# Performance work log

Hardware: AMD Instinct MI355X
Metric: run time of the kernel (lower is better)

## Reference

```python
import jax, jax.numpy as jnp
import numpy as np

K = 1024          # num_embeddings
D = 128           # embedding_dim
EMA_DECAY = 0.99
EPS = 1e-5


def setup_inputs() -> dict:
    key = jax.random.key(0)
    k1, k2, k3 = jax.random.split(key, 3)
    z = jax.random.normal(k1, (64, D, 32, 32), dtype=jnp.float32)
    codebook = jax.random.normal(k2, (K, D), dtype=jnp.float32)
    ema_count = jnp.zeros((K,), dtype=jnp.float32)
    ema_weight = jax.random.normal(k3, (K, D), dtype=jnp.float32)
    return {"z": z, "codebook": codebook, "ema_count": ema_count, "ema_weight": ema_weight}


def reference(z, codebook, ema_count, ema_weight):
    B, C, H, W = z.shape
    # flatten to [N, D] in BHWC order (matches permute(0,2,3,1).view(-1, D))
    z_flat = jnp.transpose(z, (0, 2, 3, 1)).reshape(-1, D)  # [N, D]

    # squared euclidean distances [N, K]
    distances = (
        jnp.sum(z_flat * z_flat, axis=1, keepdims=True)
        + jnp.sum(codebook * codebook, axis=1)
        - 2.0 * jnp.matmul(z_flat, codebook.T)
    )
    indices = jnp.argmin(distances, axis=1)  # [N] int

    # gather instead of one-hot @ codebook (same math)
    quantized_flat = codebook[indices]  # [N, D]
    # NOTE: faithful to original: raw view of BHWC-ordered flat buffer into z.shape
    quantized = quantized_flat.reshape(z.shape)

    # EMA statistics (no_grad in original): segment sums instead of one-hot matmuls
    encodings_sum = jax.ops.segment_sum(jnp.ones_like(indices, dtype=jnp.float32), indices, num_segments=K)
    dw = jax.ops.segment_sum(z_flat, indices, num_segments=K)  # [K, D]
    new_ema_count = EMA_DECAY * ema_count + (1.0 - EMA_DECAY) * encodings_sum
    new_ema_weight = EMA_DECAY * ema_weight + (1.0 - EMA_DECAY) * dw
    n = jnp.sum(new_ema_count)
    weights = (new_ema_count + EPS) / (n + K * EPS) * n
    new_codebook = new_ema_weight / weights[:, None]

    commitment_loss = jnp.mean((jax.lax.stop_gradient(quantized) - z) ** 2)
    codebook_loss = jnp.mean((quantized - jax.lax.stop_gradient(z)) ** 2)

    # straight-through estimator
    quantized_st = z + jax.lax.stop_gradient(quantized - z)

    idx_map = indices.reshape(B, H, W)
    return (quantized_st, idx_map, commitment_loss, codebook_loss,
            new_codebook, new_ema_count, new_ema_weight)
```

## Files before the change

kernel.cpp:

```cpp
#include <hip/hip_runtime.h>

#define NVEC 65536
#define KCB  1024
#define DIM  128
#define HW   1024
#define CHUNK 32
#define NCHUNKS (NVEC / CHUNK)

typedef __bf16 b16;
typedef b16 b16x8 __attribute__((ext_vector_type(8)));
typedef float f32x16 __attribute__((ext_vector_type(16)));

static __device__ __forceinline__ unsigned short f2bf(float f) {
  unsigned int x = __float_as_uint(f);
  unsigned int r = x + 0x7fffu + ((x >> 16) & 1u);
  return (unsigned short)(r >> 16);
}

__global__ void k_prep(const float* __restrict__ cb, const float* __restrict__ emw,
                       uint4* __restrict__ cbt, float* __restrict__ ccb,
                       double* __restrict__ cc64, float* __restrict__ out6,
                       int* __restrict__ hist, int* __restrict__ done) {
  const int t = blockIdx.x * blockDim.x + threadIdx.x;
  const int kc = t >> 11, u = t & 2047;
  const int code7 = u & 127, dch = u >> 7;
  const float* src = cb + (kc * 128 + code7) * 128 + dch * 8;
  const float4 x = *(const float4*)src;
  const float4 y = *(const float4*)(src + 4);
  uint4 o;
  o.x = (unsigned)f2bf(x.x) | ((unsigned)f2bf(x.y) << 16);
  o.y = (unsigned)f2bf(x.z) | ((unsigned)f2bf(x.w) << 16);
  o.z = (unsigned)f2bf(y.x) | ((unsigned)f2bf(y.y) << 16);
  o.w = (unsigned)f2bf(y.z) | ((unsigned)f2bf(y.w) << 16);
  cbt[t] = o;
  if (t == 0) *done = 0;
  const float4 e0 = *(const float4*)(emw + (size_t)t * 8);
  const float4 e1 = *(const float4*)(emw + (size_t)t * 8 + 4);
  *(float2*)(out6 + (size_t)t * 8 + 0) = make_float2(0.99f * e0.x, 0.99f * e0.y);
  *(float2*)(out6 + (size_t)t * 8 + 2) = make_float2(0.99f * e0.z, 0.99f * e0.w);
  *(float2*)(out6 + (size_t)t * 8 + 4) = make_float2(0.99f * e1.x, 0.99f * e1.y);
  *(float2*)(out6 + (size_t)t * 8 + 6) = make_float2(0.99f * e1.z, 0.99f * e1.w);
  if (t < KCB) hist[t] = 0;
  if (blockIdx.x < 4) {
    const int k = blockIdx.x * 256 + threadIdx.x;
    const float* row = cb + k * DIM;
    double s = 0.0;
#pragma unroll 8
    for (int j = 0; j < DIM; ++j) {
      const double v = (double)row[j];
      s = fma(v, v, s);
    }
    cc64[k] = s;
    ccb[k] = 512.f - 0.5f * (float)s;
  }
}

__global__ __launch_bounds__(256, 4) void k_argmin6(
    const float* __restrict__ z, const uint4* __restrict__ cbt,
    const float* __restrict__ ccb, const double* __restrict__ cc64,
    const float* __restrict__ cb, const float* __restrict__ emc,
    float* __restrict__ z_t, float* __restrict__ out1, int* __restrict__ hist,
    int* __restrict__ cursor, float* __restrict__ out5, float* __restrict__ ntot,
    int* __restrict__ done) {
  __shared__ __align__(16) float zs[128][65];
  __shared__ uint2 cand[64][2];
  __shared__ int isLast, wsum[4];
  __shared__ float red[4];
  uint4* Bs = (uint4*)zs;
  const int tid = threadIdx.x;
  const int l = tid & 63, wv = tid >> 6;
  const int g = l >> 5;
  const int lm = l & 31;
  const int wr = (wv & 1) * 32;
  const int wc = wv >> 1;
  const int n0 = blockIdx.x * 64;
  const int b = n0 >> 10;
  const int hwbase = n0 & (HW - 1);

  {
    const int hw4 = (tid & 15) * 4;
    const int dr = tid >> 4;
    const float* src = z + (size_t)b * 131072 + hwbase + hw4;
#pragma unroll
    for (int j = 0; j < 8; ++j) {
      const int d = dr + 16 * j;
      const float4 v = *(const float4*)(src + d * 1024);
      zs[d][hw4 + 0] = v.x; zs[d][hw4 + 1] = v.y;
      zs[d][hw4 + 2] = v.z; zs[d][hw4 + 3] = v.w;
    }
  }
  __syncthreads();

#pragma unroll
  for (int jj = 0; jj < 2; ++jj) {
    const int row = (tid >> 3) + 32 * jj;
    float* dst = z_t + ((size_t)(n0 + row)) * 128;
#pragma unroll
    for (int j = 0; j < 4; ++j) {
      const int d = (j * 8 + (tid & 7)) * 4;
      float4 v;
      v.x = zs[d + 0][row]; v.y = zs[d + 1][row];
      v.z = zs[d + 2][row]; v.w = zs[d + 3][row];
      *(float4*)(dst + d) = v;
    }
  }
  uint4 afrag[8];
  {
    const int row = wr + lm;
#pragma unroll
    for (int ks = 0; ks < 8; ++ks) {
      const int d0 = ks * 16 + g * 8;
      afrag[ks].x = (unsigned)f2bf(zs[d0 + 0][row]) | ((unsigned)f2bf(zs[d0 + 1][row]) << 16);
      afrag[ks].y = (unsigned)f2bf(zs[d0 + 2][row]) | ((unsigned)f2bf(zs[d0 + 3][row]) << 16);
      afrag[ks].z = (unsigned)f2bf(zs[d0 + 4][row]) | ((unsigned)f2bf(zs[d0 + 5][row]) << 16);
      afrag[ks].w = (unsigned)f2bf(zs[d0 + 6][row]) | ((unsigned)f2bf(zs[d0 + 7][row]) << 16);
    }
  }

  unsigned pm1[16], pm2[16];
#pragma unroll
  for (int r = 0; r < 16; ++r) { pm1[r] = 0u; pm2[r] = 0u; }

  for (int kc = 0; kc < 8; ++kc) {
    __syncthreads();
#pragma unroll
    for (int i = 0; i < 8; ++i) {
      __builtin_amdgcn_global_load_lds(&cbt[kc * 2048 + wv * 512 + i * 64 + l],
                                       &Bs[wv * 512 + i * 64], 16, 0, 0);
    }
    const float cv0 = ccb[kc * 128 + (wc * 2 + 0) * 32 + lm];
    const float cv1 = ccb[kc * 128 + (wc * 2 + 1) * 32 + lm];
    __syncthreads();

    f32x16 a0, a1;
#pragma unroll
    for (int j = 0; j < 16; ++j) { a0[j] = cv0; a1[j] = cv1; }
#pragma unroll
    for (int ks = 0; ks < 8; ++ks) {
      const b16x8 av = *reinterpret_cast<const b16x8*>(&afrag[ks]);
      const b16x8 bv0 = *reinterpret_cast<const b16x8*>(&Bs[(ks * 2 + g) * 128 + (wc * 2) * 32 + lm]);
      const b16x8 bv1 = *reinterpret_cast<const b16x8*>(&Bs[(ks * 2 + g) * 128 + (wc * 2 + 1) * 32 + lm]);
      a0 = __builtin_amdgcn_mfma_f32_32x32x16_bf16(av, bv0, a0, 0, 0, 0);
      a1 = __builtin_amdgcn_mfma_f32_32x32x16_bf16(av, bv1, a1, 0, 0, 0);
    }
    const unsigned ci0 = 1023u - (unsigned)(kc * 128 + (wc * 2) * 32 + lm);
    const unsigned ci1 = ci0 - 32u;
#pragma unroll
    for (int r = 0; r < 16; ++r) {
      {
        const unsigned uu = ((__float_as_uint(a0[r]) + 0x200u) & 0xFFFFFC00u) | ci0;
        const unsigned t = pm1[r] < uu ? pm1[r] : uu;
        pm1[r] = pm1[r] > uu ? pm1[r] : uu;
        pm2[r] = pm2[r] > t ? pm2[r] : t;
      }
      {
        const unsigned uu = ((__float_as_uint(a1[r]) + 0x200u) & 0xFFFFFC00u) | ci1;
        const unsigned t = pm1[r] < uu ? pm1[r] : uu;
        pm1[r] = pm1[r] > uu ? pm1[r] : uu;
        pm2[r] = pm2[r] > t ? pm2[r] : t;
      }
    }
  }

#pragma unroll
  for (int r = 0; r < 16; ++r) {
    unsigned u1 = pm1[r], u2 = pm2[r];
#pragma unroll
    for (int m = 1; m < 32; m <<= 1) {
      const unsigned o1 = (unsigned)__shfl_xor((int)u1, m, 64);
      const unsigned o2 = (unsigned)__shfl_xor((int)u2, m, 64);
      const unsigned s = u1 < o1 ? u1 : o1;
      u1 = u1 > o1 ? u1 : o1;
      u2 = u2 > o2 ? u2 : o2;
      u2 = u2 > s ? u2 : s;
    }
    if (lm == 0) {
      const int lrow = wr + (r & 3) + 8 * (r >> 2) + 4 * g;
      cand[lrow][wc] = make_uint2(u1, u2);
    }
  }
  __syncthreads();

  int* h = (int*)zs;
#pragma unroll
  for (int j = 0; j < 4; ++j) h[tid + 256 * j] = 0;
  __syncthreads();
  {
    const int db = l & 15, c = l >> 4;
#pragma unroll 2
    for (int it = 0; it < 16; ++it) {
      const int row = wv * 16 + it;
      const uint2 cd = cand[row][c >> 1];
      const unsigned u = (c & 1) ? cd.y : cd.x;
      int k = 1023 - (int)(u & 1023u);
      const int n = n0 + row;
      const float4* zr = (const float4*)(z_t + (size_t)n * DIM) + db * 2;
      const float4* cr = (const float4*)(cb + (size_t)k * DIM) + db * 2;
      const float4 z0 = zr[0], z1 = zr[1];
      const float4 c0 = cr[0], c1 = cr[1];
      double da = 0.0, dbb = 0.0;
      da = fma((double)z0.x, (double)c0.x, da);
      da = fma((double)z0.y, (double)c0.y, da);
      da = fma((double)z0.z, (double)c0.z, da);
      da = fma((double)z0.w, (double)c0.w, da);
      dbb = fma((double)z1.x, (double)c1.x, dbb);
      dbb = fma((double)z1.y, (double)c1.y, dbb);
      dbb = fma((double)z1.z, (double)c1.z, dbb);
      dbb = fma((double)z1.w, (double)c1.w, dbb);
      double s = da + dbb;
#pragma unroll
      for (int m = 1; m < 16; m <<= 1) s += __shfl_xor(s, m, 64);
      s = fma(-2.0, s, cc64[k]);
#pragma unroll
      for (int m = 16; m < 64; m <<= 1) {
        const double os = __shfl_xor(s, m, 64);
        const int ok = __shfl_xor(k, m, 64);
        if (os < s || (os == s && ok < k)) { s = os; k = ok; }
      }
      if (l == 0) {
        out1[n] = (float)k;
        atomicAdd(&h[k], 1);
      }
    }
  }
  __syncthreads();
#pragma unroll
  for (int j = 0; j < 4; ++j) {
    const int v = h[tid + 256 * j];
    if (v) atomicAdd(&hist[tid + 256 * j], v);
  }

  __syncthreads();
  if (tid == 0) {
    const int old = atomicAdd(done, 1);
    isLast = (old == (int)gridDim.x - 1);
  }
  __syncthreads();
  if (isLast) {
    const int i0 = tid * 4;
    const int v0 = atomicAdd(&hist[i0 + 0], 0);
    const int v1 = atomicAdd(&hist[i0 + 1], 0);
    const int v2 = atomicAdd(&hist[i0 + 2], 0);
    const int v3 = atomicAdd(&hist[i0 + 3], 0);
    const int ts = v0 + v1 + v2 + v3;
    int x = ts;
#pragma unroll
    for (int dd = 1; dd < 64; dd <<= 1) {
      const int y = __shfl_up(x, dd, 64);
      if ((tid & 63) >= dd) x += y;
    }
    if ((tid & 63) == 63) wsum[tid >> 6] = x;
    __syncthreads();
    int wb = 0;
#pragma unroll
    for (int w = 0; w < 4; ++w) wb += (w < (tid >> 6)) ? wsum[w] : 0;
    const int base = wb + x - ts;
    cursor[i0 + 0] = base;
    cursor[i0 + 1] = base + v0;
    cursor[i0 + 2] = base + v0 + v1;
    cursor[i0 + 3] = base + v0 + v1 + v2;
    const float o0 = 0.99f * emc[i0 + 0] + 0.01f * (float)v0;
    const float o1 = 0.99f * emc[i0 + 1] + 0.01f * (float)v1;
    const float o2 = 0.99f * emc[i0 + 2] + 0.01f * (float)v2;
    const float o3 = 0.99f * emc[i0 + 3] + 0.01f * (float)v3;
    out5[i0 + 0] = o0; out5[i0 + 1] = o1;
    out5[i0 + 2] = o2; out5[i0 + 3] = o3;
    float p = o0 + o1 + o2 + o3;
#pragma unroll
    for (int m = 32; m; m >>= 1) p += __shfl_xor(p, m, 64);
    if ((tid & 63) == 0) red[tid >> 6] = p;
    __syncthreads();
    if (tid == 0) *ntot = red[0] + red[1] + red[2] + red[3];
  }
}

__global__ void k_scatter(const float* __restrict__ idx_f, int* __restrict__ cursor,
                          uint2* __restrict__ ok) {
  const int n = blockIdx.x * blockDim.x + threadIdx.x;
  const int k = (int)idx_f[n];
  const int pos = atomicAdd(&cursor[k], 1);
  ok[pos] = make_uint2((unsigned)n, (unsigned)k);
}

__global__ __launch_bounds__(128) void k_chunkreduce_q(
    float* zq, const float* __restrict__ cb, const uint2* __restrict__ ok,
    float* __restrict__ out6, float* __restrict__ lossp) {
  __shared__ int so[CHUNK], sk[CHUNK];
  __shared__ float red[2];
  const int t = threadIdx.x;
  const int base = blockIdx.x * CHUNK;
  if (t < CHUNK) {
    const uint2 v = ok[base + t];
    so[t] = (int)v.x; sk[t] = (int)v.y;
  }
  __syncthreads();
  int kprev = sk[0];
  float cbv = cb[kprev * 128 + t];
  float acc = 0.f, loss = 0.f;
  int i = 0;
  while (i < CHUNK) {
    if (i + 8 <= CHUNK && sk[i] == kprev && sk[i + 7] == kprev) {
      const int n0 = so[i + 0], n1 = so[i + 1], n2 = so[i + 2], n3 = so[i + 3];
      const int n4 = so[i + 4], n5 = so[i + 5], n6 = so[i + 6], n7 = so[i + 7];
      const float v0 = zq[(size_t)n0 * 128 + t];
      const float v1 = zq[(size_t)n1 * 128 + t];
      const float v2 = zq[(size_t)n2 * 128 + t];
      const float v3 = zq[(size_t)n3 * 128 + t];
      const float v4 = zq[(size_t)n4 * 128 + t];
      const float v5 = zq[(size_t)n5 * 128 + t];
      const float v6 = zq[(size_t)n6 * 128 + t];
      const float v7 = zq[(size_t)n7 * 128 + t];
      acc += ((v0 + v1) + (v2 + v3)) + ((v4 + v5) + (v6 + v7));
      float e;
      e = cbv - v0; loss = fmaf(e, e, loss);
      e = cbv - v1; loss = fmaf(e, e, loss);
      e = cbv - v2; loss = fmaf(e, e, loss);
      e = cbv - v3; loss = fmaf(e, e, loss);
      e = cbv - v4; loss = fmaf(e, e, loss);
      e = cbv - v5; loss = fmaf(e, e, loss);
      e = cbv - v6; loss = fmaf(e, e, loss);
      e = cbv - v7; loss = fmaf(e, e, loss);
      zq[(size_t)n0 * 128 + t] = cbv; zq[(size_t)n1 * 128 + t] = cbv;
      zq[(size_t)n2 * 128 + t] = cbv; zq[(size_t)n3 * 128 + t] = cbv;
      zq[(size_t)n4 * 128 + t] = cbv; zq[(size_t)n5 * 128 + t] = cbv;
      zq[(size_t)n6 * 128 + t] = cbv; zq[(size_t)n7 * 128 + t] = cbv;
      i += 8;
    } else {
      const int kk = sk[i];
      if (kk != kprev) {
        atomicAdd(&out6[kprev * 128 + t], 0.01f * acc);
        acc = 0.f; kprev = kk;
        cbv = cb[kk * 128 + t];
      }
      const int n = so[i];
      const float v = zq[(size_t)n * 128 + t];
      acc += v;
      const float e = cbv - v; loss = fmaf(e, e, loss);
      zq[(size_t)n * 128 + t] = cbv;
      ++i;
    }
  }
  atomicAdd(&out6[kprev * 128 + t], 0.01f * acc);
#pragma unroll
  for (int m = 32; m; m >>= 1) loss += __shfl_xor(loss, m, 64);
  if ((t & 63) == 0) red[t >> 6] = loss;
  __syncthreads();
  if (t == 0) lossp[blockIdx.x] = red[0] + red[1];
}

__global__ void k_final(const float* __restrict__ out5, const float* __restrict__ out6,
                        const float* __restrict__ ntot_p, const float* __restrict__ lossp,
                        float* __restrict__ out4, float* __restrict__ out2,
                        float* __restrict__ out3) {
  __shared__ float red[4];
  const int i = blockIdx.x * blockDim.x + threadIdx.x;
  const float ntot = *ntot_p;
  const int k = i >> 7;
  const float w = (out5[k] + 1e-5f) / (ntot + KCB * 1e-5f) * ntot;
  out4[i] = out6[i] / w;
  if (blockIdx.x == 511) {
    const int t = threadIdx.x;
    float s = 0.f;
#pragma unroll
    for (int j = 0; j < NCHUNKS / 256; ++j) s += lossp[t + 256 * j];
#pragma unroll
    for (int m = 32; m; m >>= 1) s += __shfl_xor(s, m, 64);
    if ((t & 63) == 0) red[t >> 6] = s;
    __syncthreads();
    if (t == 0) {
      const float lv = (red[0] + red[1] + red[2] + red[3]) * (1.f / 8388608.f);
      *out2 = lv; *out3 = lv;
    }
  }
}

extern "C" void kernel_launch(void* const* d_in, const int* in_sizes, int n_in,
                              void* d_out, int out_size, void* d_ws, size_t ws_size,
                              hipStream_t stream) {
  (void)in_sizes; (void)n_in; (void)out_size; (void)ws_size;
  const float* z   = (const float*)d_in[0];
  const float* cb  = (const float*)d_in[1];
  const float* emc = (const float*)d_in[2];
  const float* emw = (const float*)d_in[3];
  float* out = (float*)d_out;
  float* out0 = out;
  float* out1 = out + 8388608;
  float* out2 = out + 8454144;
  float* out3 = out + 8454145;
  float* out4 = out + 8454146;
  float* out5 = out + 8585218;
  float* out6 = out + 8586242;
  float* ws = (float*)d_ws;
  uint4* cbt      = (uint4*)ws;
  uint2* okbuf    = (uint2*)(ws + 65536);
  float* ccb      = ws + 327680;
  int* hist       = (int*)(ws + 328704);
  int* cursor     = (int*)(ws + 329728);
  float* ntot     = ws + 330752;
  int* done       = (int*)(ws + 330756);
  float* lossp    = ws + 331776;
  double* cc64    = (double*)(ws + 333824);
  float* z_t = out0;

  hipLaunchKernelGGL(k_prep, dim3(64), dim3(256), 0, stream, cb, emw, cbt, ccb,
                     cc64, out6, hist, done);
  hipLaunchKernelGGL(k_argmin6, dim3(NVEC / 64), dim3(256), 0, stream,
                     z, cbt, ccb, cc64, cb, emc, z_t, out1, hist, cursor,
                     out5, ntot, done);
  hipLaunchKernelGGL(k_scatter, dim3(NVEC / 256), dim3(256), 0, stream, out1, cursor,
                     okbuf);
  hipLaunchKernelGGL(k_chunkreduce_q, dim3(NCHUNKS), dim3(128), 0, stream,
                     z_t, cb, okbuf, out6, lossp);
  hipLaunchKernelGGL(k_final, dim3(512), dim3(256), 0, stream, out5, out6, ntot,
                     lossp, out4, out2, out3);
}
```

Baseline: 126.5 us.

## Double-buffer codebook chunks in LDS and widen argmin blocks to 128 rows

Each argmin block now covers 128 vectors with 512 threads, and the codebook-chunk loads into LDS are double-buffered. The next chunk's global_load_lds is issued while the current chunk's MFMA runs, which removes one barrier per iteration and the load stall at the start of each chunk. Each codebook chunk is also reused across twice as many rows. The cost is a larger shared-memory footprint (about 66KB for zs), which may cut resident blocks per CU. The tail scan and histogram code are adapted to 8 waves.

```diff
diff --git a/kernel.cpp b/kernel.cpp
--- a/kernel.cpp
+++ b/kernel.cpp
@@ -55,31 +55,32 @@
   }
 }
 
-__global__ __launch_bounds__(256, 4) void k_argmin6(
+__global__ __launch_bounds__(512, 4) void k_argmin8(
     const float* __restrict__ z, const uint4* __restrict__ cbt,
     const float* __restrict__ ccb, const double* __restrict__ cc64,
     const float* __restrict__ cb, const float* __restrict__ emc,
     float* __restrict__ z_t, float* __restrict__ out1, int* __restrict__ hist,
     int* __restrict__ cursor, float* __restrict__ out5, float* __restrict__ ntot,
     int* __restrict__ done) {
-  __shared__ __align__(16) float zs[128][65];
-  __shared__ uint2 cand[64][2];
-  __shared__ int isLast, wsum[4];
-  __shared__ float red[4];
-  uint4* Bs = (uint4*)zs;
+  __shared__ __align__(16) float zs[128][129];
+  __shared__ uint2 cand[128][2];
+  __shared__ int isLast, wsum[8];
+  __shared__ float red[8];
+  uint4* BsA = (uint4*)zs;
+  uint4* BsB = ((uint4*)zs) + 2048;
   const int tid = threadIdx.x;
   const int l = tid & 63, wv = tid >> 6;
   const int g = l >> 5;
   const int lm = l & 31;
-  const int wr = (wv & 1) * 32;
-  const int wc = wv >> 1;
-  const int n0 = blockIdx.x * 64;
+  const int wr = (wv & 3) * 32;
+  const int ch = wv >> 2;
+  const int n0 = blockIdx.x * 128;
   const int b = n0 >> 10;
   const int hwbase = n0 & (HW - 1);
 
   {
-    const int hw4 = (tid & 15) * 4;
-    const int dr = tid >> 4;
+    const int hw4 = (tid & 31) * 4;
+    const int dr = tid >> 5;
     const float* src = z + (size_t)b * 131072 + hwbase + hw4;
 #pragma unroll
     for (int j = 0; j < 8; ++j) {
@@ -93,7 +94,7 @@
 
 #pragma unroll
   for (int jj = 0; jj < 2; ++jj) {
-    const int row = (tid >> 3) + 32 * jj;
+    const int row = (tid >> 3) + 64 * jj;
     float* dst = z_t + ((size_t)(n0 + row)) * 128;
 #pragma unroll
     for (int j = 0; j < 4; ++j) {
@@ -121,29 +122,38 @@
 #pragma unroll
   for (int r = 0; r < 16; ++r) { pm1[r] = 0u; pm2[r] = 0u; }
 
-  for (int kc = 0; kc < 8; ++kc) {
+  __syncthreads();
+#pragma unroll
+  for (int i = 0; i < 4; ++i) {
+    __builtin_amdgcn_global_load_lds(&cbt[wv * 256 + i * 64 + l],
+                                     &BsA[wv * 256 + i * 64], 16, 0, 0);
+  }
+
+  for (int c = 0; c < 8; ++c) {
     __syncthreads();
-#pragma unroll
-    for (int i = 0; i < 8; ++i) {
-      __builtin_amdgcn_global_load_lds(&cbt[kc * 2048 + wv * 512 + i * 64 + l],
-                                       &Bs[wv * 512 + i * 64], 16, 0, 0);
-    }
-    const float cv0 = ccb[kc * 128 + (wc * 2 + 0) * 32 + lm];
-    const float cv1 = ccb[kc * 128 + (wc * 2 + 1) * 32 + lm];
-    __syncthreads();
-
+    const uint4* cur = (c & 1) ? BsB : BsA;
+    uint4* nxt = (c & 1) ? BsA : BsB;
+    if (c < 7) {
+#pragma unroll
+      for (int i = 0; i < 4; ++i) {
+        __builtin_amdgcn_global_load_lds(&cbt[(c + 1) * 2048 + wv * 256 + i * 64 + l],
+                                         &nxt[wv * 256 + i * 64], 16, 0, 0);
+      }
+    }
+    const float cv0 = ccb[c * 128 + (ch * 2 + 0) * 32 + lm];
+    const float cv1 = ccb[c * 128 + (ch * 2 + 1) * 32 + lm];
     f32x16 a0, a1;
 #pragma unroll
     for (int j = 0; j < 16; ++j) { a0[j] = cv0; a1[j] = cv1; }
 #pragma unroll
     for (int ks = 0; ks < 8; ++ks) {
       const b16x8 av = *reinterpret_cast<const b16x8*>(&afrag[ks]);
-      const b16x8 bv0 = *reinterpret_cast<const b16x8*>(&Bs[(ks * 2 + g) * 128 + (wc * 2) * 32 + lm]);
-      const b16x8 bv1 = *reinterpret_cast<const b16x8*>(&Bs[(ks * 2 + g) * 128 + (wc * 2 + 1) * 32 + lm]);
+      const b16x8 bv0 = *reinterpret_cast<const b16x8*>(&cur[(ks * 2 + g) * 128 + (ch * 2) * 32 + lm]);
+      const b16x8 bv1 = *reinterpret_cast<const b16x8*>(&cur[(ks * 2 + g) * 128 + (ch * 2 + 1) * 32 + lm]);
       a0 = __builtin_amdgcn_mfma_f32_32x32x16_bf16(av, bv0, a0, 0, 0, 0);
       a1 = __builtin_amdgcn_mfma_f32_32x32x16_bf16(av, bv1, a1, 0, 0, 0);
     }
-    const unsigned ci0 = 1023u - (unsigned)(kc * 128 + (wc * 2) * 32 + lm);
+    const unsigned ci0 = 1023u - (unsigned)(c * 128 + (ch * 2) * 32 + lm);
     const unsigned ci1 = ci0 - 32u;
 #pragma unroll
     for (int r = 0; r < 16; ++r) {
@@ -176,14 +186,14 @@
     }
     if (lm == 0) {
       const int lrow = wr + (r & 3) + 8 * (r >> 2) + 4 * g;
-      cand[lrow][wc] = make_uint2(u1, u2);
+      cand[lrow][ch] = make_uint2(u1, u2);
     }
   }
   __syncthreads();
 
   int* h = (int*)zs;
 #pragma unroll
-  for (int j = 0; j < 4; ++j) h[tid + 256 * j] = 0;
+  for (int j = 0; j < 2; ++j) h[tid + 512 * j] = 0;
   __syncthreads();
   {
     const int db = l & 15, c = l >> 4;
@@ -225,9 +235,9 @@
   }
   __syncthreads();
 #pragma unroll
-  for (int j = 0; j < 4; ++j) {
-    const int v = h[tid + 256 * j];
-    if (v) atomicAdd(&hist[tid + 256 * j], v);
+  for (int j = 0; j < 2; ++j) {
+    const int v = h[tid + 512 * j];
+    if (v) atomicAdd(&hist[tid + 512 * j], v);
   }
 
   __syncthreads();
@@ -237,12 +247,10 @@
   }
   __syncthreads();
   if (isLast) {
-    const int i0 = tid * 4;
+    const int i0 = tid * 2;
     const int v0 = atomicAdd(&hist[i0 + 0], 0);
     const int v1 = atomicAdd(&hist[i0 + 1], 0);
-    const int v2 = atomicAdd(&hist[i0 + 2], 0);
-    const int v3 = atomicAdd(&hist[i0 + 3], 0);
-    const int ts = v0 + v1 + v2 + v3;
+    const int ts = v0 + v1;
     int x = ts;
 #pragma unroll
     for (int dd = 1; dd < 64; dd <<= 1) {
@@ -253,24 +261,24 @@
     __syncthreads();
     int wb = 0;
 #pragma unroll
-    for (int w = 0; w < 4; ++w) wb += (w < (tid >> 6)) ? wsum[w] : 0;
+    for (int w = 0; w < 8; ++w) wb += (w < (tid >> 6)) ? wsum[w] : 0;
     const int base = wb + x - ts;
     cursor[i0 + 0] = base;
     cursor[i0 + 1] = base + v0;
-    cursor[i0 + 2] = base + v0 + v1;
-    cursor[i0 + 3] = base + v0 + v1 + v2;
     const float o0 = 0.99f * emc[i0 + 0] + 0.01f * (float)v0;
     const float o1 = 0.99f * emc[i0 + 1] + 0.01f * (float)v1;
-    const float o2 = 0.99f * emc[i0 + 2] + 0.01f * (float)v2;
-    const float o3 = 0.99f * emc[i0 + 3] + 0.01f * (float)v3;
     out5[i0 + 0] = o0; out5[i0 + 1] = o1;
-    out5[i0 + 2] = o2; out5[i0 + 3] = o3;
-    float p = o0 + o1 + o2 + o3;
+    float p = o0 + o1;
 #pragma unroll
     for (int m = 32; m; m >>= 1) p += __shfl_xor(p, m, 64);
     if ((tid & 63) == 0) red[tid >> 6] = p;
     __syncthreads();
-    if (tid == 0) *ntot = red[0] + red[1] + red[2] + red[3];
+    if (tid == 0) {
+      float s = 0.f;
+#pragma unroll
+      for (int w = 0; w < 8; ++w) s += red[w];
+      *ntot = s;
+    }
   }
 }
 
@@ -404,7 +412,7 @@
 
   hipLaunchKernelGGL(k_prep, dim3(64), dim3(256), 0, stream, cb, emw, cbt, ccb,
                      cc64, out6, hist, done);
-  hipLaunchKernelGGL(k_argmin6, dim3(NVEC / 64), dim3(256), 0, stream,
+  hipLaunchKernelGGL(k_argmin8, dim3(NVEC / 128), dim3(512), 0, stream,
                      z, cbt, ccb, cc64, cb, emc, z_t, out1, hist, cursor,
                      out5, ntot, done);
   hipLaunchKernelGGL(k_scatter, dim3(NVEC / 256), dim3(256), 0, stream, out1, cursor,
```

Measured after the change: 124.2 us. About the same (-1.8%).
